# Performance work log

Hardware: AMD Instinct MI355X
Metric: run time of the kernel (lower is better)

The kernel has to match this reference:

```python
import jax, jax.numpy as jnp
import numpy as np

N_NODES = 10000
N_EDGES = 320000
IN_FEATS = 512
N_UNITS = 256
OUT_FEATS = 64
N_LAYERS = 6  # number of hidden GCNConv layers feeding the JK max


def setup_inputs() -> dict:
    key = jax.random.key(0)
    ks = jax.random.split(key, 8)
    h = jax.random.normal(ks[0], (N_NODES, IN_FEATS), dtype=jnp.float32)
    edge_index = jax.random.randint(ks[1], (2, N_EDGES), 0, N_NODES, dtype=jnp.int64)
    # learned parameters (glorot-ish scale)
    W0 = jax.random.normal(ks[2], (IN_FEATS, N_UNITS), dtype=jnp.float32) * (1.0 / np.sqrt(IN_FEATS))
    b0 = jnp.zeros((N_UNITS,), dtype=jnp.float32)
    Wh = jax.random.normal(ks[3], (N_LAYERS - 1, N_UNITS, N_UNITS), dtype=jnp.float32) * (1.0 / np.sqrt(N_UNITS))
    bh = jnp.zeros((N_LAYERS - 1, N_UNITS), dtype=jnp.float32)
    Wo = jax.random.normal(ks[4], (N_UNITS, OUT_FEATS), dtype=jnp.float32) * (1.0 / np.sqrt(N_UNITS))
    bo = jnp.zeros((OUT_FEATS,), dtype=jnp.float32)
    return {"h": h, "edge_index": edge_index, "W0": W0, "b0": b0,
            "Wh": Wh, "bh": bh, "Wo": Wo, "bo": bo}


def reference(h, edge_index, W0, b0, Wh, bh, Wo, bo):
    src = edge_index[0]
    dst = edge_index[1]
    n = h.shape[0]

    def conv_plain(x, W, b):
        # GCNConv with normalize=False: plain sum aggregation over edges, no self-loops
        m = x @ W                                   # [N, d]
        agg = jax.ops.segment_sum(m[src], dst, num_segments=n)
        return jax.nn.relu(agg + b)

    outs = []
    x = conv_plain(h, W0, b0)
    outs.append(x)
    for i in range(Wh.shape[0]):  # dropout is identity in eval mode
        x = conv_plain(x, Wh[i], bh[i])
        outs.append(x)

    # jumping-knowledge max aggregation over layer outputs
    x = jnp.max(jnp.stack(outs, axis=0), axis=0)    # [N, n_units]

    # final GCNConv with normalize=True (symmetric GCN norm, self-loops added)
    m = x @ Wo                                      # [N, out_feats]
    ones = jnp.ones(dst.shape, dtype=m.dtype)
    deg = jax.ops.segment_sum(ones, dst, num_segments=n) + 1.0  # +1 self loop
    dinv = deg ** -0.5
    coef = dinv[src] * dinv[dst]                    # [E]
    agg = jax.ops.segment_sum(m[src] * coef[:, None], dst, num_segments=n)
    agg = agg + m / deg[:, None] + bo               # self-loop term 1/deg_i
    return jax.nn.log_softmax(agg, axis=-1)
```

## Files before the change

kernel.cpp:

```cpp
#include <hip/hip_runtime.h>
#include <math.h>

#define N_NODES 10000
#define N_EDGES 320000
#define IN_FEATS 512
#define N_UNITS 256
#define OUT_FEATS 64
#define N_HID 5

typedef __attribute__((ext_vector_type(8))) short bf16x8;
typedef __attribute__((ext_vector_type(4))) float f32x4;

__device__ __forceinline__ unsigned short f2bf(float f) {
    union { float f; unsigned int u; } c; c.f = f;
    unsigned int u = c.u + 0x7FFFu + ((c.u >> 16) & 1u);
    return (unsigned short)(u >> 16);
}
__device__ __forceinline__ float bf2f(unsigned short b) {
    union { unsigned int u; float f; } c; c.u = ((unsigned int)b) << 16;
    return c.f;
}


__global__ void k_hist(const int* __restrict__ dst, int* __restrict__ deg) {
    int e = blockIdx.x * blockDim.x + threadIdx.x;
    if (e < N_EDGES) atomicAdd(&deg[dst[e]], 1);
}

__global__ __launch_bounds__(1024) void k_scan(const int* __restrict__ deg,
                                               int* __restrict__ row_ptr,
                                               int* __restrict__ cursor,
                                               float* __restrict__ dinv,
                                               float* __restrict__ invdeg) {
    __shared__ int wsum[16];
    const int PER = 10;
    int t = threadIdx.x;
    int lane = t & 63, wid = t >> 6;
    int base = t * PER;

    int v[PER];
    int s = 0;
#pragma unroll
    for (int j = 0; j < PER; ++j) {
        int i = base + j;
        int d = (i < N_NODES) ? deg[i] : 0;
        v[j] = s;
        s += d;
    }
    int inc = s;
#pragma unroll
    for (int off = 1; off < 64; off <<= 1) {
        int y = __shfl_up(inc, off);
        if (lane >= off) inc += y;
    }
    if (lane == 63) wsum[wid] = inc;
    __syncthreads();
    if (wid == 0) {
        int w = (lane < 16) ? wsum[lane] : 0;
#pragma unroll
        for (int off = 1; off < 16; off <<= 1) {
            int y = __shfl_up(w, off);
            if (lane >= off) w += y;
        }
        if (lane < 16) wsum[lane] = w;
    }
    __syncthreads();
    int wave_excl = (wid == 0) ? 0 : wsum[wid - 1];
    int thread_excl = wave_excl + (inc - s);

#pragma unroll
    for (int j = 0; j < PER; ++j) {
        int i = base + j;
        if (i < N_NODES) {
            int rp = thread_excl + v[j];
            row_ptr[i] = rp;
            cursor[i]  = rp;
            int d = ((j + 1 < PER) ? v[j + 1] : s) - v[j];
            float dd = (float)(d + 1);
            dinv[i]   = rsqrtf(dd);
            invdeg[i] = 1.0f / dd;
        }
    }
    if (t == 1023) row_ptr[N_NODES] = thread_excl + s;
}

__global__ void k_fill(const int* __restrict__ src, const int* __restrict__ dst,
                       int* __restrict__ cursor, int* __restrict__ csr_src) {
    int e = blockIdx.x * blockDim.x + threadIdx.x;
    if (e < N_EDGES) {
        int p = atomicAdd(&cursor[dst[e]], 1);
        csr_src[p] = src[e];
    }
}


__global__ void k_cvth(const float* __restrict__ h, unsigned short* __restrict__ hb) {
    int t = blockIdx.x * blockDim.x + threadIdx.x;
    if (t < N_NODES * IN_FEATS / 4) {
        float4 v = reinterpret_cast<const float4*>(h)[t];
        ushort4 o;
        o.x = f2bf(v.x); o.y = f2bf(v.y); o.z = f2bf(v.z); o.w = f2bf(v.w);
        reinterpret_cast<ushort4*>(hb)[t] = o;
    }
}

__global__ void k_cvtw(const float* __restrict__ W0, const float* __restrict__ Wh,
                       const float* __restrict__ Wo,
                       unsigned short* __restrict__ W0t, unsigned short* __restrict__ Wht,
                       unsigned short* __restrict__ Wot) {
    int t = blockIdx.x * blockDim.x + threadIdx.x;
    const int S0 = IN_FEATS * N_UNITS;
    const int SH = N_HID * N_UNITS * N_UNITS;
    const int SO = N_UNITS * OUT_FEATS;
    if (t < S0) {
        int k = t >> 8, n = t & 255;
        W0t[(size_t)n * IN_FEATS + k] = f2bf(W0[t]);
    } else if (t < S0 + SH) {
        int u = t - S0;
        int l = u >> 16;
        int r = u & 65535;
        int k = r >> 8, n = r & 255;
        Wht[(size_t)l * 65536 + (size_t)n * N_UNITS + k] = f2bf(Wh[u]);
    } else if (t < S0 + SH + SO) {
        int u = t - S0 - SH;
        int k = u >> 6, n = u & 63;
        Wot[(size_t)n * N_UNITS + k] = f2bf(Wo[u]);
    }
}


template<bool OUT_BF16>
__global__ __launch_bounds__(256) void k_mgemm(const unsigned short* __restrict__ A,
                                               const unsigned short* __restrict__ Bt,
                                               void* __restrict__ Cv,
                                               const int M, const int K, const int Nld) {
    constexpr int BM = 64, BN = 64, BK = 32;
    __shared__ unsigned short As[BM * BK];
    __shared__ unsigned short Bs[BN * BK];

    const int tid  = threadIdx.x;
    const int wid  = tid >> 6;
    const int lane = tid & 63;
    const int wr   = wid >> 1;
    const int wc   = wid & 1;
    const int brow = blockIdx.x * BM;
    const int bcol = blockIdx.y * BN;

    const int lr = lane & 15;
    const int lk = lane >> 4;

    const int row = tid >> 2;
    const int slot = tid & 3;

    f32x4 acc[2][2];
#pragma unroll
    for (int m = 0; m < 2; ++m)
#pragma unroll
        for (int n = 0; n < 2; ++n)
            acc[m][n] = (f32x4){0.f, 0.f, 0.f, 0.f};

    int gra = brow + row; if (gra >= M) gra = M - 1;
    const unsigned short* gpa = A + (size_t)gra * K + slot * 8;
    const unsigned short* gpb = Bt + (size_t)(bcol + row) * K + slot * 8;

    for (int k0 = 0; k0 < K; k0 += BK) {
        __builtin_amdgcn_global_load_lds(
            (const __attribute__((address_space(1))) void*)(gpa + k0),
            (__attribute__((address_space(3))) void*)(As + tid * 8), 16, 0, 0);
        __builtin_amdgcn_global_load_lds(
            (const __attribute__((address_space(1))) void*)(gpb + k0),
            (__attribute__((address_space(3))) void*)(Bs + tid * 8), 16, 0, 0);
        __syncthreads();

        bf16x8 af[2], bfr[2];
#pragma unroll
        for (int m = 0; m < 2; ++m)
            af[m] = *reinterpret_cast<const bf16x8*>(&As[(wr * 32 + m * 16 + lr) * BK + lk * 8]);
#pragma unroll
        for (int n = 0; n < 2; ++n)
            bfr[n] = *reinterpret_cast<const bf16x8*>(&Bs[(wc * 32 + n * 16 + lr) * BK + lk * 8]);
#pragma unroll
        for (int m = 0; m < 2; ++m)
#pragma unroll
            for (int n = 0; n < 2; ++n)
                acc[m][n] = __builtin_amdgcn_mfma_f32_16x16x32_bf16(af[m], bfr[n], acc[m][n], 0, 0, 0);
        __syncthreads();
    }

#pragma unroll
    for (int m = 0; m < 2; ++m) {
#pragma unroll
        for (int r = 0; r < 4; ++r) {
            int orow = brow + wr * 32 + m * 16 + lk * 4 + r;
            if (orow < M) {
#pragma unroll
                for (int n = 0; n < 2; ++n) {
                    int ocol = bcol + wc * 32 + n * 16 + lr;
                    float v = acc[m][n][r];
                    if (OUT_BF16)
                        ((unsigned short*)Cv)[(size_t)orow * Nld + ocol] = f2bf(v);
                    else
                        ((float*)Cv)[(size_t)orow * Nld + ocol] = v;
                }
            }
        }
    }
}


__global__ __launch_bounds__(64) void k_agg(const unsigned short* __restrict__ m,
                                            const int* __restrict__ row_ptr,
                                            const int* __restrict__ csr_src,
                                            const float* __restrict__ bias,
                                            unsigned short* __restrict__ x_out,
                                            unsigned short* __restrict__ jk,
                                            int init_jk) {
    int n = blockIdx.x;
    int lane = threadIdx.x;
    int s = row_ptr[n], e = row_ptr[n + 1];
    const uint2* mv = (const uint2*)m;

    float a0 = 0.f, a1 = 0.f, a2 = 0.f, a3 = 0.f;
    int i = s;
    for (; i + 3 < e; i += 4) {
        int s0 = csr_src[i], s1 = csr_src[i + 1], s2 = csr_src[i + 2], s3 = csr_src[i + 3];
        uint2 u0 = mv[(size_t)s0 * 64 + lane];
        uint2 u1 = mv[(size_t)s1 * 64 + lane];
        uint2 u2 = mv[(size_t)s2 * 64 + lane];
        uint2 u3 = mv[(size_t)s3 * 64 + lane];
        a0 += bf2f(u0.x & 0xffff) + bf2f(u1.x & 0xffff) + bf2f(u2.x & 0xffff) + bf2f(u3.x & 0xffff);
        a1 += bf2f(u0.x >> 16)    + bf2f(u1.x >> 16)    + bf2f(u2.x >> 16)    + bf2f(u3.x >> 16);
        a2 += bf2f(u0.y & 0xffff) + bf2f(u1.y & 0xffff) + bf2f(u2.y & 0xffff) + bf2f(u3.y & 0xffff);
        a3 += bf2f(u0.y >> 16)    + bf2f(u1.y >> 16)    + bf2f(u2.y >> 16)    + bf2f(u3.y >> 16);
    }
    for (; i < e; ++i) {
        uint2 u = mv[(size_t)csr_src[i] * 64 + lane];
        a0 += bf2f(u.x & 0xffff);
        a1 += bf2f(u.x >> 16);
        a2 += bf2f(u.y & 0xffff);
        a3 += bf2f(u.y >> 16);
    }

    float4 b = ((const float4*)bias)[lane];
    unsigned int h0 = f2bf(fmaxf(a0 + b.x, 0.f));
    unsigned int h1 = f2bf(fmaxf(a1 + b.y, 0.f));
    unsigned int h2 = f2bf(fmaxf(a2 + b.z, 0.f));
    unsigned int h3 = f2bf(fmaxf(a3 + b.w, 0.f));
    uint2 o;
    o.x = h0 | (h1 << 16);
    o.y = h2 | (h3 << 16);

    size_t idx = (size_t)n * 64 + lane;
    ((uint2*)x_out)[idx] = o;
    if (init_jk) {
        ((uint2*)jk)[idx] = o;
    } else {
        uint2 j = ((const uint2*)jk)[idx];
        unsigned int j0 = j.x & 0xffff, j1 = j.x >> 16, j2 = j.y & 0xffff, j3 = j.y >> 16;
        j0 = (h0 > j0) ? h0 : j0;
        j1 = (h1 > j1) ? h1 : j1;
        j2 = (h2 > j2) ? h2 : j2;
        j3 = (h3 > j3) ? h3 : j3;
        uint2 w;
        w.x = j0 | (j1 << 16);
        w.y = j2 | (j3 << 16);
        ((uint2*)jk)[idx] = w;
    }
}


__global__ __launch_bounds__(256) void k_final(const unsigned short* __restrict__ mf,
                                               const int* __restrict__ row_ptr,
                                               const int* __restrict__ csr_src,
                                               const float* __restrict__ dinv,
                                               const float* __restrict__ invdeg,
                                               const float* __restrict__ bo,
                                               float* __restrict__ out) {
    int wid  = threadIdx.x >> 6;
    int lane = threadIdx.x & 63;
    int n = blockIdx.x * 4 + wid;
    if (n >= N_NODES) return;

    int s = row_ptr[n], e = row_ptr[n + 1];
    float acc = 0.f;
    int i = s;
    for (; i + 3 < e; i += 4) {
        int s0 = csr_src[i], s1 = csr_src[i + 1], s2 = csr_src[i + 2], s3 = csr_src[i + 3];
        acc += bf2f(mf[(size_t)s0 * OUT_FEATS + lane]) * dinv[s0];
        acc += bf2f(mf[(size_t)s1 * OUT_FEATS + lane]) * dinv[s1];
        acc += bf2f(mf[(size_t)s2 * OUT_FEATS + lane]) * dinv[s2];
        acc += bf2f(mf[(size_t)s3 * OUT_FEATS + lane]) * dinv[s3];
    }
    for (; i < e; ++i) {
        int sr = csr_src[i];
        acc += bf2f(mf[(size_t)sr * OUT_FEATS + lane]) * dinv[sr];
    }
    acc *= dinv[n];
    acc += bf2f(mf[(size_t)n * OUT_FEATS + lane]) * invdeg[n] + bo[lane];

    float mx = acc;
#pragma unroll
    for (int off = 32; off; off >>= 1) mx = fmaxf(mx, __shfl_xor(mx, off));
    float ex = __expf(acc - mx);
    float sum = ex;
#pragma unroll
    for (int off = 32; off; off >>= 1) sum += __shfl_xor(sum, off);
    out[(size_t)n * OUT_FEATS + lane] = acc - mx - __logf(sum);
}


extern "C" void kernel_launch(void* const* d_in, const int* in_sizes, int n_in,
                              void* d_out, int out_size, void* d_ws, size_t ws_size,
                              hipStream_t stream) {
    const float* h  = (const float*)d_in[0];
    const int*   ei = (const int*)d_in[1];
    const float* W0 = (const float*)d_in[2];
    const float* b0 = (const float*)d_in[3];
    const float* Wh = (const float*)d_in[4];
    const float* bh = (const float*)d_in[5];
    const float* Wo = (const float*)d_in[6];
    const float* bo = (const float*)d_in[7];

    const int* src = ei;
    const int* dst = ei + N_EDGES;

    char* p = (char*)d_ws;
    auto carve = [&](size_t bytes) {
        char* r = p;
        p += (bytes + 255) & ~(size_t)255;
        return r;
    };
    int*   deg     = (int*)  carve(N_NODES * 4);
    int*   row_ptr = (int*)  carve((N_NODES + 1) * 4);
    int*   cursor  = (int*)  carve(N_NODES * 4);
    int*   csr_src = (int*)  carve(N_EDGES * 4);
    float* dinv    = (float*)carve(N_NODES * 4);
    float* invdeg  = (float*)carve(N_NODES * 4);
    unsigned short* hb  = (unsigned short*)carve((size_t)N_NODES * IN_FEATS * 2);
    unsigned short* W0t = (unsigned short*)carve((size_t)IN_FEATS * N_UNITS * 2);
    unsigned short* Wht = (unsigned short*)carve((size_t)N_HID * N_UNITS * N_UNITS * 2);
    unsigned short* Wot = (unsigned short*)carve((size_t)N_UNITS * OUT_FEATS * 2);
    unsigned short* m   = (unsigned short*)carve((size_t)N_NODES * N_UNITS * 2);
    unsigned short* x   = (unsigned short*)carve((size_t)N_NODES * N_UNITS * 2);
    unsigned short* jk  = (unsigned short*)carve((size_t)N_NODES * N_UNITS * 2);
    unsigned short* mf  = (unsigned short*)carve((size_t)N_NODES * OUT_FEATS * 2);

    hipMemsetAsync(deg, 0, N_NODES * 4, stream);
    k_hist<<<(N_EDGES + 255) / 256, 256, 0, stream>>>(dst, deg);
    k_scan<<<1, 1024, 0, stream>>>(deg, row_ptr, cursor, dinv, invdeg);
    k_fill<<<(N_EDGES + 255) / 256, 256, 0, stream>>>(src, dst, cursor, csr_src);

    k_cvth<<<(N_NODES * IN_FEATS / 4 + 255) / 256, 256, 0, stream>>>(h, hb);
    {
        int total = IN_FEATS * N_UNITS + N_HID * N_UNITS * N_UNITS + N_UNITS * OUT_FEATS;
        k_cvtw<<<(total + 255) / 256, 256, 0, stream>>>(W0, Wh, Wo, W0t, Wht, Wot);
    }

    const int GBM = (N_NODES + 63) / 64;

    {
        dim3 g(GBM, N_UNITS / 64);
        k_mgemm<true><<<g, 256, 0, stream>>>(hb, W0t, m, N_NODES, IN_FEATS, N_UNITS);
    }
    k_agg<<<N_NODES, 64, 0, stream>>>(m, row_ptr, csr_src, b0, x, jk, 1);

    for (int l = 0; l < N_HID; ++l) {
        dim3 g(GBM, N_UNITS / 64);
        k_mgemm<true><<<g, 256, 0, stream>>>(x, Wht + (size_t)l * N_UNITS * N_UNITS,
                                             m, N_NODES, N_UNITS, N_UNITS);
        k_agg<<<N_NODES, 64, 0, stream>>>(m, row_ptr, csr_src, bh + (size_t)l * N_UNITS,
                                          x, jk, 0);
    }

    {
        dim3 g(GBM, 1);
        k_mgemm<true><<<g, 256, 0, stream>>>(jk, Wot, mf, N_NODES, N_UNITS, OUT_FEATS);
    }
    k_final<<<(N_NODES + 3) / 4, 256, 0, stream>>>(mf, row_ptr, csr_src, dinv, invdeg,
                                                   bo, (float*)d_out);
}
```

Baseline: 264.2 us.

## Fuse setup kernels, double-buffer and swizzle GEMM, add full-K GEMM, widen aggregation

Merges the degree histogram and the input and weight bf16 conversions into one setup launch. Double-buffers the generic GEMM's LDS tiles with an XOR swizzle to reduce bank conflicts. Adds a GEMM for K=256 that loads the whole K slice into LDS with a single barrier. Aggregation now packs 8 nodes per 256-thread block and has each lane load 16-byte vectors. The aim is fewer launches, less synchronization and better memory-access efficiency, at the cost of 64 KB of LDS per block in the new GEMM, which may limit occupancy.

```diff
diff --git a/kernel.cpp b/kernel.cpp
--- a/kernel.cpp
+++ b/kernel.cpp
@@ -16,16 +16,51 @@
     unsigned int u = c.u + 0x7FFFu + ((c.u >> 16) & 1u);
     return (unsigned short)(u >> 16);
 }
-__device__ __forceinline__ float bf2f(unsigned short b) {
-    union { unsigned int u; float f; } c; c.u = ((unsigned int)b) << 16;
+__device__ __forceinline__ float bf2f(unsigned int b) {
+    union { unsigned int u; float f; } c; c.u = (b & 0xffffu) << 16;
     return c.f;
 }
 
 
-__global__ void k_hist(const int* __restrict__ dst, int* __restrict__ deg) {
-    int e = blockIdx.x * blockDim.x + threadIdx.x;
-    if (e < N_EDGES) atomicAdd(&deg[dst[e]], 1);
-}
+__global__ void k_setup(const int* __restrict__ dst, int* __restrict__ deg,
+                        const float* __restrict__ h, unsigned short* __restrict__ hb,
+                        const float* __restrict__ W0, const float* __restrict__ Wh,
+                        const float* __restrict__ Wo,
+                        unsigned short* __restrict__ W0t, unsigned short* __restrict__ Wht,
+                        unsigned short* __restrict__ Wot) {
+    const int R1 = N_EDGES;
+    const int R2 = N_NODES * IN_FEATS / 4;
+    const int S0 = IN_FEATS * N_UNITS;
+    const int SH = N_HID * N_UNITS * N_UNITS;
+    const int SO = N_UNITS * OUT_FEATS;
+    int t = blockIdx.x * blockDim.x + threadIdx.x;
+    if (t < R1) {
+        atomicAdd(&deg[dst[t]], 1);
+    } else if (t < R1 + R2) {
+        int u = t - R1;
+        float4 v = reinterpret_cast<const float4*>(h)[u];
+        ushort4 o;
+        o.x = f2bf(v.x); o.y = f2bf(v.y); o.z = f2bf(v.z); o.w = f2bf(v.w);
+        reinterpret_cast<ushort4*>(hb)[u] = o;
+    } else {
+        int u = t - R1 - R2;
+        if (u < S0) {
+            int k = u >> 8, n = u & 255;
+            W0t[(size_t)n * IN_FEATS + k] = f2bf(W0[u]);
+        } else if (u < S0 + SH) {
+            int w = u - S0;
+            int l = w >> 16;
+            int r = w & 65535;
+            int k = r >> 8, n = r & 255;
+            Wht[(size_t)l * 65536 + (size_t)n * N_UNITS + k] = f2bf(Wh[w]);
+        } else if (u < S0 + SH + SO) {
+            int w = u - S0 - SH;
+            int k = w >> 6, n = w & 63;
+            Wot[(size_t)n * N_UNITS + k] = f2bf(Wo[w]);
+        }
+    }
+}
+
 
 __global__ __launch_bounds__(1024) void k_scan(const int* __restrict__ deg,
                                                int* __restrict__ row_ptr,
@@ -94,49 +129,13 @@
 }
 
 
-__global__ void k_cvth(const float* __restrict__ h, unsigned short* __restrict__ hb) {
-    int t = blockIdx.x * blockDim.x + threadIdx.x;
-    if (t < N_NODES * IN_FEATS / 4) {
-        float4 v = reinterpret_cast<const float4*>(h)[t];
-        ushort4 o;
-        o.x = f2bf(v.x); o.y = f2bf(v.y); o.z = f2bf(v.z); o.w = f2bf(v.w);
-        reinterpret_cast<ushort4*>(hb)[t] = o;
-    }
-}
-
-__global__ void k_cvtw(const float* __restrict__ W0, const float* __restrict__ Wh,
-                       const float* __restrict__ Wo,
-                       unsigned short* __restrict__ W0t, unsigned short* __restrict__ Wht,
-                       unsigned short* __restrict__ Wot) {
-    int t = blockIdx.x * blockDim.x + threadIdx.x;
-    const int S0 = IN_FEATS * N_UNITS;
-    const int SH = N_HID * N_UNITS * N_UNITS;
-    const int SO = N_UNITS * OUT_FEATS;
-    if (t < S0) {
-        int k = t >> 8, n = t & 255;
-        W0t[(size_t)n * IN_FEATS + k] = f2bf(W0[t]);
-    } else if (t < S0 + SH) {
-        int u = t - S0;
-        int l = u >> 16;
-        int r = u & 65535;
-        int k = r >> 8, n = r & 255;
-        Wht[(size_t)l * 65536 + (size_t)n * N_UNITS + k] = f2bf(Wh[u]);
-    } else if (t < S0 + SH + SO) {
-        int u = t - S0 - SH;
-        int k = u >> 6, n = u & 63;
-        Wot[(size_t)n * N_UNITS + k] = f2bf(Wo[u]);
-    }
-}
-
-
-template<bool OUT_BF16>
 __global__ __launch_bounds__(256) void k_mgemm(const unsigned short* __restrict__ A,
                                                const unsigned short* __restrict__ Bt,
-                                               void* __restrict__ Cv,
+                                               unsigned short* __restrict__ C,
                                                const int M, const int K, const int Nld) {
     constexpr int BM = 64, BN = 64, BK = 32;
-    __shared__ unsigned short As[BM * BK];
-    __shared__ unsigned short Bs[BN * BK];
+    __shared__ unsigned short As[2][BM * BK];
+    __shared__ unsigned short Bs[2][BN * BK];
 
     const int tid  = threadIdx.x;
     const int wid  = tid >> 6;
@@ -149,8 +148,13 @@
     const int lr = lane & 15;
     const int lk = lane >> 4;
 
-    const int row = tid >> 2;
+    const int row  = tid >> 2;
     const int slot = tid & 3;
+    const int sslot = slot ^ ((row >> 1) & 3);
+
+    int gra = brow + row; if (gra >= M) gra = M - 1;
+    const unsigned short* gpa = A + (size_t)gra * K + sslot * 8;
+    const unsigned short* gpb = Bt + (size_t)(bcol + row) * K + sslot * 8;
 
     f32x4 acc[2][2];
 #pragma unroll
@@ -159,26 +163,35 @@
         for (int n = 0; n < 2; ++n)
             acc[m][n] = (f32x4){0.f, 0.f, 0.f, 0.f};
 
-    int gra = brow + row; if (gra >= M) gra = M - 1;
-    const unsigned short* gpa = A + (size_t)gra * K + slot * 8;
-    const unsigned short* gpb = Bt + (size_t)(bcol + row) * K + slot * 8;
-
-    for (int k0 = 0; k0 < K; k0 += BK) {
-        __builtin_amdgcn_global_load_lds(
-            (const __attribute__((address_space(1))) void*)(gpa + k0),
-            (__attribute__((address_space(3))) void*)(As + tid * 8), 16, 0, 0);
-        __builtin_amdgcn_global_load_lds(
-            (const __attribute__((address_space(1))) void*)(gpb + k0),
-            (__attribute__((address_space(3))) void*)(Bs + tid * 8), 16, 0, 0);
-        __syncthreads();
+#define STAGE(buf, k0)                                                                      \
+    do {                                                                                    \
+        __builtin_amdgcn_global_load_lds(                                                   \
+            (const __attribute__((address_space(1))) void*)(gpa + (k0)),                    \
+            (__attribute__((address_space(3))) void*)(&As[(buf)][tid * 8]), 16, 0, 0);      \
+        __builtin_amdgcn_global_load_lds(                                                   \
+            (const __attribute__((address_space(1))) void*)(gpb + (k0)),                    \
+            (__attribute__((address_space(3))) void*)(&Bs[(buf)][tid * 8]), 16, 0, 0);      \
+    } while (0)
+
+    STAGE(0, 0);
+    __syncthreads();
+
+    const int nk = K / BK;
+    for (int kt = 0; kt < nk; ++kt) {
+        const int cur = kt & 1;
+        if (kt + 1 < nk) STAGE(cur ^ 1, (kt + 1) * BK);
 
         bf16x8 af[2], bfr[2];
 #pragma unroll
-        for (int m = 0; m < 2; ++m)
-            af[m] = *reinterpret_cast<const bf16x8*>(&As[(wr * 32 + m * 16 + lr) * BK + lk * 8]);
-#pragma unroll
-        for (int n = 0; n < 2; ++n)
-            bfr[n] = *reinterpret_cast<const bf16x8*>(&Bs[(wc * 32 + n * 16 + lr) * BK + lk * 8]);
+        for (int m = 0; m < 2; ++m) {
+            int ra = wr * 32 + m * 16 + lr;
+            af[m] = *reinterpret_cast<const bf16x8*>(&As[cur][ra * BK + (lk ^ ((ra >> 1) & 3)) * 8]);
+        }
+#pragma unroll
+        for (int n = 0; n < 2; ++n) {
+            int rb = wc * 32 + n * 16 + lr;
+            bfr[n] = *reinterpret_cast<const bf16x8*>(&Bs[cur][rb * BK + (lk ^ ((rb >> 1) & 3)) * 8]);
+        }
 #pragma unroll
         for (int m = 0; m < 2; ++m)
 #pragma unroll
@@ -186,6 +199,7 @@
                 acc[m][n] = __builtin_amdgcn_mfma_f32_16x16x32_bf16(af[m], bfr[n], acc[m][n], 0, 0, 0);
         __syncthreads();
     }
+#undef STAGE
 
 #pragma unroll
     for (int m = 0; m < 2; ++m) {
@@ -196,11 +210,7 @@
 #pragma unroll
                 for (int n = 0; n < 2; ++n) {
                     int ocol = bcol + wc * 32 + n * 16 + lr;
-                    float v = acc[m][n][r];
-                    if (OUT_BF16)
-                        ((unsigned short*)Cv)[(size_t)orow * Nld + ocol] = f2bf(v);
-                    else
-                        ((float*)Cv)[(size_t)orow * Nld + ocol] = v;
+                    C[(size_t)orow * Nld + ocol] = f2bf(acc[m][n][r]);
                 }
             }
         }
@@ -208,63 +218,149 @@
 }
 
 
-__global__ __launch_bounds__(64) void k_agg(const unsigned short* __restrict__ m,
-                                            const int* __restrict__ row_ptr,
-                                            const int* __restrict__ csr_src,
-                                            const float* __restrict__ bias,
-                                            unsigned short* __restrict__ x_out,
-                                            unsigned short* __restrict__ jk,
-                                            int init_jk) {
-    int n = blockIdx.x;
-    int lane = threadIdx.x;
+__global__ __launch_bounds__(256) void k_wgemm(const unsigned short* __restrict__ A,
+                                               const unsigned short* __restrict__ Bt,
+                                               unsigned short* __restrict__ C,
+                                               const int M, const int Nld) {
+    constexpr int K = 256;
+    __shared__ unsigned short As[64 * K];
+    __shared__ unsigned short Bs[64 * K];
+
+    const int tid  = threadIdx.x;
+    const int wid  = tid >> 6;
+    const int lane = tid & 63;
+    const int lr   = lane & 15;
+    const int lk   = lane >> 4;
+    const int brow = blockIdx.x * 64;
+    const int bcol = blockIdx.y * 64;
+
+#pragma unroll
+    for (int p = 0; p < 8; ++p) {
+        int i = p * 256 + tid;
+        int row = i >> 5, s = i & 31;
+        int gr = brow + row; if (gr >= M) gr = M - 1;
+        const unsigned short* gp = A + (size_t)gr * K + ((s ^ (row & 7)) * 8);
+        __builtin_amdgcn_global_load_lds(
+            (const __attribute__((address_space(1))) void*)gp,
+            (__attribute__((address_space(3))) void*)(As + i * 8), 16, 0, 0);
+    }
+#pragma unroll
+    for (int p = 0; p < 8; ++p) {
+        int i = p * 256 + tid;
+        int row = i >> 5, s = i & 31;
+        const unsigned short* gp = Bt + (size_t)(bcol + row) * K + ((s ^ (row & 7)) * 8);
+        __builtin_amdgcn_global_load_lds(
+            (const __attribute__((address_space(1))) void*)gp,
+            (__attribute__((address_space(3))) void*)(Bs + i * 8), 16, 0, 0);
+    }
+    __syncthreads();
+
+    f32x4 acc[4];
+#pragma unroll
+    for (int n = 0; n < 4; ++n) acc[n] = (f32x4){0.f, 0.f, 0.f, 0.f};
+
+    const int ra = (wid << 4) + lr;
+    const unsigned short* Arow = As + ra * K;
+    const int e = lr & 7;
+#pragma unroll
+    for (int kk = 0; kk < 8; ++kk) {
+        bf16x8 av = *reinterpret_cast<const bf16x8*>(&Arow[(((kk << 2) + lk) ^ e) * 8]);
+#pragma unroll
+        for (int n = 0; n < 4; ++n) {
+            const unsigned short* Brow = Bs + ((n << 4) + lr) * K;
+            bf16x8 bv = *reinterpret_cast<const bf16x8*>(&Brow[(((kk << 2) + lk) ^ e) * 8]);
+            acc[n] = __builtin_amdgcn_mfma_f32_16x16x32_bf16(av, bv, acc[n], 0, 0, 0);
+        }
+    }
+
+#pragma unroll
+    for (int n = 0; n < 4; ++n) {
+#pragma unroll
+        for (int r = 0; r < 4; ++r) {
+            int orow = brow + (wid << 4) + (lk << 2) + r;
+            if (orow < M) {
+                int ocol = bcol + (n << 4) + lr;
+                C[(size_t)orow * Nld + ocol] = f2bf(acc[n][r]);
+            }
+        }
+    }
+}
+
+
+__global__ __launch_bounds__(256) void k_agg(const unsigned short* __restrict__ m,
+                                             const int* __restrict__ row_ptr,
+                                             const int* __restrict__ csr_src,
+                                             const float* __restrict__ bias,
+                                             unsigned short* __restrict__ x_out,
+                                             unsigned short* __restrict__ jk,
+                                             int init_jk) {
+    int half = threadIdx.x >> 5;
+    int lane = threadIdx.x & 31;
+    int n = blockIdx.x * 8 + half;
     int s = row_ptr[n], e = row_ptr[n + 1];
-    const uint2* mv = (const uint2*)m;
-
-    float a0 = 0.f, a1 = 0.f, a2 = 0.f, a3 = 0.f;
+    const uint4* mv = (const uint4*)m;
+
+    float a[8];
+#pragma unroll
+    for (int j = 0; j < 8; ++j) a[j] = 0.f;
+
+#define ACC8(u)                                        \
+    do {                                               \
+        a[0] += bf2f((u).x); a[1] += bf2f((u).x >> 16);\
+        a[2] += bf2f((u).y); a[3] += bf2f((u).y >> 16);\
+        a[4] += bf2f((u).z); a[5] += bf2f((u).z >> 16);\
+        a[6] += bf2f((u).w); a[7] += bf2f((u).w >> 16);\
+    } while (0)
+
     int i = s;
     for (; i + 3 < e; i += 4) {
         int s0 = csr_src[i], s1 = csr_src[i + 1], s2 = csr_src[i + 2], s3 = csr_src[i + 3];
-        uint2 u0 = mv[(size_t)s0 * 64 + lane];
-        uint2 u1 = mv[(size_t)s1 * 64 + lane];
-        uint2 u2 = mv[(size_t)s2 * 64 + lane];
-        uint2 u3 = mv[(size_t)s3 * 64 + lane];
-        a0 += bf2f(u0.x & 0xffff) + bf2f(u1.x & 0xffff) + bf2f(u2.x & 0xffff) + bf2f(u3.x & 0xffff);
-        a1 += bf2f(u0.x >> 16)    + bf2f(u1.x >> 16)    + bf2f(u2.x >> 16)    + bf2f(u3.x >> 16);
-        a2 += bf2f(u0.y & 0xffff) + bf2f(u1.y & 0xffff) + bf2f(u2.y & 0xffff) + bf2f(u3.y & 0xffff);
-        a3 += bf2f(u0.y >> 16)    + bf2f(u1.y >> 16)    + bf2f(u2.y >> 16)    + bf2f(u3.y >> 16);
+        uint4 u0 = mv[(size_t)s0 * 32 + lane];
+        uint4 u1 = mv[(size_t)s1 * 32 + lane];
+        uint4 u2 = mv[(size_t)s2 * 32 + lane];
+        uint4 u3 = mv[(size_t)s3 * 32 + lane];
+        ACC8(u0); ACC8(u1); ACC8(u2); ACC8(u3);
     }
     for (; i < e; ++i) {
-        uint2 u = mv[(size_t)csr_src[i] * 64 + lane];
-        a0 += bf2f(u.x & 0xffff);
-        a1 += bf2f(u.x >> 16);
-        a2 += bf2f(u.y & 0xffff);
-        a3 += bf2f(u.y >> 16);
-    }
-
-    float4 b = ((const float4*)bias)[lane];
-    unsigned int h0 = f2bf(fmaxf(a0 + b.x, 0.f));
-    unsigned int h1 = f2bf(fmaxf(a1 + b.y, 0.f));
-    unsigned int h2 = f2bf(fmaxf(a2 + b.z, 0.f));
-    unsigned int h3 = f2bf(fmaxf(a3 + b.w, 0.f));
-    uint2 o;
-    o.x = h0 | (h1 << 16);
-    o.y = h2 | (h3 << 16);
-
-    size_t idx = (size_t)n * 64 + lane;
-    ((uint2*)x_out)[idx] = o;
+        uint4 u = mv[(size_t)csr_src[i] * 32 + lane];
+        ACC8(u);
+    }
+#undef ACC8
+
+    float4 b0 = ((const float4*)bias)[lane * 2];
+    float4 b1 = ((const float4*)bias)[lane * 2 + 1];
+    unsigned int hh[8];
+    hh[0] = f2bf(fmaxf(a[0] + b0.x, 0.f));
+    hh[1] = f2bf(fmaxf(a[1] + b0.y, 0.f));
+    hh[2] = f2bf(fmaxf(a[2] + b0.z, 0.f));
+    hh[3] = f2bf(fmaxf(a[3] + b0.w, 0.f));
+    hh[4] = f2bf(fmaxf(a[4] + b1.x, 0.f));
+    hh[5] = f2bf(fmaxf(a[5] + b1.y, 0.f));
+    hh[6] = f2bf(fmaxf(a[6] + b1.z, 0.f));
+    hh[7] = f2bf(fmaxf(a[7] + b1.w, 0.f));
+    uint4 o;
+    o.x = hh[0] | (hh[1] << 16);
+    o.y = hh[2] | (hh[3] << 16);
+    o.z = hh[4] | (hh[5] << 16);
+    o.w = hh[6] | (hh[7] << 16);
+
+    size_t idx = (size_t)n * 32 + lane;
+    ((uint4*)x_out)[idx] = o;
     if (init_jk) {
-        ((uint2*)jk)[idx] = o;
+        ((uint4*)jk)[idx] = o;
     } else {
-        uint2 j = ((const uint2*)jk)[idx];
-        unsigned int j0 = j.x & 0xffff, j1 = j.x >> 16, j2 = j.y & 0xffff, j3 = j.y >> 16;
-        j0 = (h0 > j0) ? h0 : j0;
-        j1 = (h1 > j1) ? h1 : j1;
-        j2 = (h2 > j2) ? h2 : j2;
-        j3 = (h3 > j3) ? h3 : j3;
-        uint2 w;
-        w.x = j0 | (j1 << 16);
-        w.y = j2 | (j3 << 16);
-        ((uint2*)jk)[idx] = w;
+        uint4 j = ((const uint4*)jk)[idx];
+        auto mx2 = [](unsigned int nw, unsigned int od) {
+            unsigned int lo_n = nw & 0xffffu, lo_o = od & 0xffffu;
+            unsigned int hi_n = nw >> 16,     hi_o = od >> 16;
+            unsigned int lo = lo_n > lo_o ? lo_n : lo_o;
+            unsigned int hi = hi_n > hi_o ? hi_n : hi_o;
+            return lo | (hi << 16);
+        };
+        uint4 w;
+        w.x = mx2(o.x, j.x); w.y = mx2(o.y, j.y);
+        w.z = mx2(o.z, j.z); w.w = mx2(o.w, j.w);
+        ((uint4*)jk)[idx] = w;
     }
 }
 
@@ -346,35 +442,34 @@
     unsigned short* mf  = (unsigned short*)carve((size_t)N_NODES * OUT_FEATS * 2);
 
     hipMemsetAsync(deg, 0, N_NODES * 4, stream);
-    k_hist<<<(N_EDGES + 255) / 256, 256, 0, stream>>>(dst, deg);
+    {
+        const int total = N_EDGES + N_NODES * IN_FEATS / 4 +
+                          IN_FEATS * N_UNITS + N_HID * N_UNITS * N_UNITS + N_UNITS * OUT_FEATS;
+        k_setup<<<(total + 255) / 256, 256, 0, stream>>>(dst, deg, h, hb, W0, Wh, Wo,
+                                                         W0t, Wht, Wot);
+    }
     k_scan<<<1, 1024, 0, stream>>>(deg, row_ptr, cursor, dinv, invdeg);
     k_fill<<<(N_EDGES + 255) / 256, 256, 0, stream>>>(src, dst, cursor, csr_src);
 
-    k_cvth<<<(N_NODES * IN_FEATS / 4 + 255) / 256, 256, 0, stream>>>(h, hb);
-    {
-        int total = IN_FEATS * N_UNITS + N_HID * N_UNITS * N_UNITS + N_UNITS * OUT_FEATS;
-        k_cvtw<<<(total + 255) / 256, 256, 0, stream>>>(W0, Wh, Wo, W0t, Wht, Wot);
-    }
-
     const int GBM = (N_NODES + 63) / 64;
 
     {
         dim3 g(GBM, N_UNITS / 64);
-        k_mgemm<true><<<g, 256, 0, stream>>>(hb, W0t, m, N_NODES, IN_FEATS, N_UNITS);
-    }
-    k_agg<<<N_NODES, 64, 0, stream>>>(m, row_ptr, csr_src, b0, x, jk, 1);
+        k_mgemm<<<g, 256, 0, stream>>>(hb, W0t, m, N_NODES, IN_FEATS, N_UNITS);
+    }
+    k_agg<<<N_NODES / 8, 256, 0, stream>>>(m, row_ptr, csr_src, b0, x, jk, 1);
 
     for (int l = 0; l < N_HID; ++l) {
         dim3 g(GBM, N_UNITS / 64);
-        k_mgemm<true><<<g, 256, 0, stream>>>(x, Wht + (size_t)l * N_UNITS * N_UNITS,
-                                             m, N_NODES, N_UNITS, N_UNITS);
-        k_agg<<<N_NODES, 64, 0, stream>>>(m, row_ptr, csr_src, bh + (size_t)l * N_UNITS,
-                                          x, jk, 0);
+        k_wgemm<<<g, 256, 0, stream>>>(x, Wht + (size_t)l * N_UNITS * N_UNITS, m,
+                                       N_NODES, N_UNITS);
+        k_agg<<<N_NODES / 8, 256, 0, stream>>>(m, row_ptr, csr_src, bh + (size_t)l * N_UNITS,
+                                               x, jk, 0);
     }
 
     {
         dim3 g(GBM, 1);
-        k_mgemm<true><<<g, 256, 0, stream>>>(jk, Wot, mf, N_NODES, N_UNITS, OUT_FEATS);
+        k_wgemm<<<g, 256, 0, stream>>>(jk, Wot, mf, N_NODES, OUT_FEATS);
     }
     k_final<<<(N_NODES + 3) / 4, 256, 0, stream>>>(mf, row_ptr, csr_src, dinv, invdeg,
                                                    bo, (float*)d_out);
```

Measured after the change: 258.1 us. 1.02x faster.
